# Kernel tuning notes

Measured on AMD Instinct MI355X. Metric: run time of the kernel, lower is better.

The kernel has to match this reference:

```python
import jax, jax.numpy as jnp
import numpy as np

B, L, V, E, M, H = 64, 256, 50000, 300, 50, 256
HD = H // 2  # per-direction LSTM hidden
C1, C2 = 1.0, 0.1


def _reverse_padded(x, lens):
    # reverse each [L, ...] sequence within its valid length; padded tail -> 0
    Ln = x.shape[1]
    idx = lens[:, None] - 1 - jnp.arange(Ln)[None, :]
    ok = idx >= 0
    idxc = jnp.clip(idx, 0, Ln - 1)
    out = jnp.take_along_axis(x, idxc[:, :, None], axis=1)
    return out * ok[:, :, None].astype(x.dtype)


def _lstm_dir(x, valid, w_ih, w_hh, b_ih, b_hh):
    # x: [B, L, D], valid: [B, L] bool. PyTorch gate order i, f, g, o.
    Bn = x.shape[0]
    Hh = w_hh.shape[1]
    xs = jnp.einsum('bld,hd->blh', x, w_ih) + b_ih  # precompute input projection
    xsT = xs.transpose(1, 0, 2)  # [L, B, 4H]
    vT = valid.T  # [L, B]

    def step(carry, inp):
        h, c = carry
        g_in, v = inp
        g = g_in + h @ w_hh.T + b_hh
        i, f, gg, o = jnp.split(g, 4, axis=1)
        c_new = jax.nn.sigmoid(f) * c + jax.nn.sigmoid(i) * jnp.tanh(gg)
        h_new = jax.nn.sigmoid(o) * jnp.tanh(c_new)
        vm = v[:, None]
        return (jnp.where(vm, h_new, h), jnp.where(vm, c_new, c)), jnp.where(vm, h_new, 0.0)

    init = (jnp.zeros((Bn, Hh), x.dtype), jnp.zeros((Bn, Hh), x.dtype))
    _, outs = jax.lax.scan(step, init, (xsT, vT))
    return outs.transpose(1, 0, 2)  # [B, L, Hh], zeros past each len (like pad_packed)


def _forward(sents, masks, labels, lens, word_embed, mask_embed,
             w_ih_f, w_hh_f, b_ih_f, b_hh_f, w_ih_b, w_hh_b, b_ih_b, b_hh_b,
             feat2tri_w, feat2tri_b, transitions, feat2label_w, feat2label_b):
    valid = jnp.arange(L)[None, :] < lens[:, None]  # [B, L]
    # SimpleCat (dropout is identity at eval)
    x = jnp.concatenate([word_embed[sents], mask_embed[masks]], axis=2)  # [B, L, E+M]
    # biLSTM (packed semantics: outputs zero past len)
    hf = _lstm_dir(x, valid, w_ih_f, w_hh_f, b_ih_f, b_hh_f)
    hb = _reverse_padded(_lstm_dir(_reverse_padded(x, lens), valid, w_ih_b, w_hh_b, b_ih_b, b_hh_b), lens)
    context = jnp.concatenate([hf, hb], axis=2)  # [B, L, H]
    # masked target average pooling, broadcast-add back
    mf = masks.astype(context.dtype)
    tavg = jnp.sum(mf[:, :, None] * context, axis=1) / jnp.sum(mf, axis=1)[:, None]
    context = context + tavg[:, None, :]
    # emission scores for the 2-state linear CRF
    emit = jnp.einsum('blh,th->blt', context, feat2tri_w) + feat2tri_b  # [B, L, 2]
    emitT = emit.transpose(1, 0, 2)  # [L, B, 2]
    vT = valid.T  # [L, B]

    # batched CRF forward (alpha), frozen past each len
    def astep(alpha, inp):
        e, v = inp
        a_new = e + jax.nn.logsumexp(alpha[:, :, None] + transitions[None], axis=1)
        alpha = jnp.where(v[:, None], a_new, alpha)
        return alpha, alpha

    alpha0 = emitT[0]
    alpha_last, alphas_rest = jax.lax.scan(astep, alpha0, (emitT[1:], vT[1:]))
    alphas = jnp.concatenate([alpha0[None], alphas_rest], axis=0)  # [L, B, 2]
    logZ = jax.nn.logsumexp(alpha_last, axis=1)  # [B]

    # batched CRF backward (beta); beta[len-1] = 0, frozen past len
    def bstep(beta, inp):
        e_next, v_next = inp
        b_new = jax.nn.logsumexp(transitions[None] + (e_next + beta)[:, None, :], axis=2)
        beta = jnp.where(v_next[:, None], b_new, beta)
        return beta, beta

    beta_init = jnp.zeros((B, 2), context.dtype)
    _, betas_rev = jax.lax.scan(bstep, beta_init, (emitT[1:][::-1], vT[1:][::-1]))
    betas = jnp.concatenate([betas_rev[::-1], beta_init[None]], axis=0)  # [L, B, 2]

    marg = jnp.exp(alphas + betas - logZ[None, :, None]) * vT[:, :, None]  # [L, B, 2]
    sp = marg[:, :, 1].T  # select_polarity, [B, L], zero past len
    sent_v = jnp.einsum('bl,blh->bh', sp, context)
    label_scores = sent_v @ feat2label_w.T + feat2label_b  # [B, 3]
    logp = jax.nn.log_softmax(label_scores, axis=1)
    cls_loss = -jnp.mean(logp[jnp.arange(B), labels])
    s_prob_norm = jnp.mean(jnp.sum(sp, axis=1))  # L1 norm of nonneg marginals
    pena = jax.nn.relu(transitions[1, 0] - transitions[0, 0]) + jax.nn.relu(transitions[0, 1] - transitions[1, 1])
    norm_pen = C1 * pena + C2 * s_prob_norm
    return jnp.stack([cls_loss, norm_pen])


def setup_inputs() -> dict:
    key = jax.random.key(0)
    ks = jax.random.split(key, 20)
    s = 0.1
    sents = jax.random.randint(ks[0], (B, L), 0, V)
    lens = jnp.sort(jax.random.randint(ks[1], (B,), 32, L + 1))[::-1]
    masks = jnp.zeros((B, L), jnp.int32).at[:, :8].set(jax.random.randint(ks[2], (B, 8), 0, 2)).at[:, 0].set(1)
    labels = jax.random.randint(ks[3], (B,), 0, 3)
    D = E + M
    return {
        'sents': sents, 'masks': masks, 'labels': labels, 'lens': lens,
        'word_embed': jax.random.normal(ks[4], (V, E)) * s,
        'mask_embed': jax.random.normal(ks[5], (2, M)) * s,
        'w_ih_f': jax.random.normal(ks[6], (4 * HD, D)) * s,
        'w_hh_f': jax.random.normal(ks[7], (4 * HD, HD)) * s,
        'b_ih_f': jnp.zeros((4 * HD,)), 'b_hh_f': jnp.zeros((4 * HD,)),
        'w_ih_b': jax.random.normal(ks[8], (4 * HD, D)) * s,
        'w_hh_b': jax.random.normal(ks[9], (4 * HD, HD)) * s,
        'b_ih_b': jnp.zeros((4 * HD,)), 'b_hh_b': jnp.zeros((4 * HD,)),
        'feat2tri_w': jax.random.normal(ks[10], (2, H)) * s,
        'feat2tri_b': jnp.zeros((2,)),
        'transitions': jax.random.normal(ks[11], (2, 2)) * s,
        'feat2label_w': jax.random.normal(ks[12], (3, H)) * s,
        'feat2label_b': jnp.zeros((3,)),
    }


def reference(sents, masks, labels, lens, word_embed, mask_embed,
              w_ih_f, w_hh_f, b_ih_f, b_hh_f, w_ih_b, w_hh_b, b_ih_b, b_hh_b,
              feat2tri_w, feat2tri_b, transitions, feat2label_w, feat2label_b):
    return _forward(sents, masks, labels, lens, word_embed, mask_embed,
                    w_ih_f, w_hh_f, b_ih_f, b_hh_f, w_ih_b, w_hh_b, b_ih_b, b_hh_b,
                    feat2tri_w, feat2tri_b, transitions, feat2label_w, feat2label_b)
```

## Files before the change

kernel.cpp:

```cpp
#include <hip/hip_runtime.h>
#include <hip/hip_bf16.h>

#define Bq 64
#define Lq 256
#define Dq 350
#define HDq 128
#define Hq 256
#define G4 512

typedef unsigned short u16;
typedef unsigned int u32;
typedef __attribute__((ext_vector_type(8))) short bf16x8;
typedef __attribute__((ext_vector_type(4))) float f32x4;

__device__ __forceinline__ float bf2f(u16 u) {
    return __uint_as_float(((u32)u) << 16);
}
__device__ __forceinline__ u16 f2bf(float f) {
    __hip_bfloat16 h = __float2bfloat16(f);
    return *(u16*)&h;
}
__device__ __forceinline__ float bflo(u32 u) {
    return __uint_as_float(u << 16);
}
__device__ __forceinline__ float bfhi(u32 u) {
    return __uint_as_float(u & 0xffff0000u);
}
__device__ __forceinline__ float loadf(const void* p, long i, int f32) {
    return f32 ? ((const float*)p)[i] : bf2f(((const u16*)p)[i]);
}
__device__ __forceinline__ float pick8(uint4 q, int i) {
    u32 w = (i >> 1) == 0 ? q.x : (i >> 1) == 1 ? q.y : (i >> 1) == 2 ? q.z : q.w;
    return (i & 1) ? bfhi(w) : bflo(w);
}
__device__ __forceinline__ float fsigm(float x) {
    return 1.f / (1.f + __expf(-x));
}
__device__ __forceinline__ float ftanh(float x) {
    return 1.f - 2.f / (__expf(2.f * x) + 1.f);
}
__device__ __forceinline__ float lse2(float x, float y) {
    float m = fmaxf(x, y);
    return m + logf(expf(x - m) + expf(y - m));
}
__device__ __forceinline__ float lse2f(float x, float y) {
    float m = fmaxf(x, y);
    return m + __logf(__expf(x - m) + __expf(y - m));
}
__device__ __forceinline__ int hswz(int m, int k) {
    return m * 128 + ((((k >> 3) + m) & 15) << 3) + (k & 7);
}
__device__ __forceinline__ u32 pack2(float lo, float hi) {
    return ((u32)f2bf(hi) << 16) | (u32)f2bf(lo);
}

__global__ void detect_kernel(const void* we, int* flag) {
    if (threadIdx.x == 0 && blockIdx.x == 0) {
        const u16* p = (const u16*)we;
        int big = 0;
        for (int i = 0; i < 256; ++i) {
            float a = fabsf(bf2f(p[i]));
            if (!(a < 2.f)) big++;
        }
        *flag = (big > 16) ? 1 : 0;
    }
}

#define LDA 40

__global__ __launch_bounds__(256) void gemm_xs_kernel(
    const int* __restrict__ sents, const int* __restrict__ masks,
    const int* __restrict__ lens,
    const void* __restrict__ word_embed,
    const void* __restrict__ mask_embed,
    const void* __restrict__ w_ih_f, const void* __restrict__ w_ih_b,
    const void* __restrict__ b_ih_f, const void* __restrict__ b_hh_f,
    const void* __restrict__ b_ih_b, const void* __restrict__ b_hh_b,
    const int* __restrict__ flag,
    u16* __restrict__ xsF)
{
    __shared__ __align__(16) u16 As[128 * LDA];
    __shared__ __align__(16) u16 Bs[128 * LDA];
    __shared__ int rowS[128];
    __shared__ int rowM[128];

    int f32 = *flag;
    int tid = threadIdx.x;
    int mBase = blockIdx.y * 128;
    int jGlob = blockIdx.x * 128;
    int dir = jGlob >> 9;
    int jj = jGlob & 511;
    const void* w_ih = dir ? w_ih_b : w_ih_f;
    const void* b_ih = dir ? b_ih_b : b_ih_f;
    const void* b_hh = dir ? b_hh_b : b_hh_f;

    int b = mBase >> 8;
    int posBase = mBase & 255;
    int len = lens[b];

    if (tid < 128) {
        int i = mBase + tid;
        rowS[tid] = sents[i] * 300;
        rowM[tid] = masks[i] * 50;
    }
    int wv = tid >> 6, lane = tid & 63;
    int quad = lane >> 4, col = lane & 15;
    int mS = tid >> 4;
    int k2S = (tid & 15) << 1;
    f32x4 acc[2][8] = {};
    __syncthreads();

    for (int kt = 0; kt < 11; ++kt) {
        int k0 = kt * 32;
        u32 aR[8], bR[8];
        if (f32) {
#pragma unroll
            for (int e = 0; e < 8; ++e) {
                int m = mS + e * 16;
                int gk = k0 + k2S;
                float2 v = make_float2(0.f, 0.f);
                if (gk < 300)
                    v = *(const float2*)((const float*)word_embed + rowS[m] + gk);
                else if (gk < 350)
                    v = *(const float2*)((const float*)mask_embed + rowM[m] + gk - 300);
                aR[e] = pack2(v.x, v.y);
                float2 w2 = make_float2(0.f, 0.f);
                if (gk < 350)
                    w2 = *(const float2*)((const float*)w_ih + (long)(jj + m) * 350 + gk);
                bR[e] = pack2(w2.x, w2.y);
            }
        } else {
#pragma unroll
            for (int e = 0; e < 8; ++e) {
                int m = mS + e * 16;
                int gk = k0 + k2S;
                u32 v = 0;
                if (gk < 300)
                    v = *(const u32*)((const u16*)word_embed + rowS[m] + gk);
                else if (gk < 350)
                    v = *(const u32*)((const u16*)mask_embed + rowM[m] + gk - 300);
                aR[e] = v;
                u32 w2 = 0;
                if (gk < 350)
                    w2 = *(const u32*)((const u16*)w_ih + (long)(jj + m) * 350 + gk);
                bR[e] = w2;
            }
        }
        __syncthreads();
#pragma unroll
        for (int e = 0; e < 8; ++e) {
            int m = mS + e * 16;
            *(u32*)&As[m * LDA + k2S] = aR[e];
            *(u32*)&Bs[m * LDA + k2S] = bR[e];
        }
        __syncthreads();
        bf16x8 af[2], bfr[8];
#pragma unroll
        for (int mt = 0; mt < 2; ++mt)
            af[mt] = *(const bf16x8*)&As[(wv * 32 + mt * 16 + col) * LDA + quad * 8];
#pragma unroll
        for (int nt = 0; nt < 8; ++nt)
            bfr[nt] = *(const bf16x8*)&Bs[(nt * 16 + col) * LDA + quad * 8];
#pragma unroll
        for (int mt = 0; mt < 2; ++mt)
#pragma unroll
            for (int nt = 0; nt < 8; ++nt)
                acc[mt][nt] = __builtin_amdgcn_mfma_f32_16x16x32_bf16(
                    af[mt], bfr[nt], acc[mt][nt], 0, 0, 0);
    }

    int bgv = b >> 2, quadv = b & 3;
#pragma unroll
    for (int nt = 0; nt < 8; ++nt) {
        int ng = jj + nt * 16 + col;
        float bias = loadf(b_ih, ng, f32) + loadf(b_hh, ng, f32);
        int g = ng >> 7, dd = ng & 127;
        int wvx = dd >> 4, colv = dd & 15;
        int row = ((dir * 16 + bgv) * 8 + wvx) * 4 + g;
        int lanev = quadv * 16 + colv;
#pragma unroll
        for (int mt = 0; mt < 2; ++mt)
#pragma unroll
            for (int r = 0; r < 4; ++r) {
                int pos = posBase + wv * 32 + mt * 16 + quad * 4 + r;
                int s = dir ? (len - 1 - pos) : pos;
                if (s >= 0) {
                    long idxe = ((long)(row * 32 + (s >> 3))) * 512
                                + lanev * 8 + (s & 7);
                    xsF[idxe] = f2bf(acc[mt][nt][r] + bias);
                }
            }
    }
}

__global__ __launch_bounds__(512, 1) void lstm_mfma_kernel(
    const u16* __restrict__ xsF,
    const void* __restrict__ w_hh_f, const void* __restrict__ w_hh_b,
    const int* __restrict__ lens, const int* __restrict__ flag,
    u16* __restrict__ context)
{
    int f32 = *flag;
    int blk = blockIdx.x;
    int dir = blk >> 4, bg = blk & 15;
    int tid = threadIdx.x;
    int w = tid >> 6, lane = tid & 63;
    int quad = lane >> 4, col = lane & 15;
    const void* w_hh = dir ? w_hh_b : w_hh_f;

    __shared__ __align__(16) u16 hbuf[2][16 * 128];
    __shared__ __align__(16) u16 hist[16 * 512];
    __shared__ int len_s[4];
    __shared__ int maxlen_s;

    if (tid < 4) len_s[tid] = lens[bg * 4 + tid];
    for (int i = tid; i < 2 * 16 * 128; i += 512) ((u16*)hbuf)[i] = 0;
    __syncthreads();
    if (tid == 0) {
        int mx = 0;
        for (int m = 0; m < 4; ++m) mx = max(mx, len_s[m]);
        maxlen_s = mx;
    }
    for (int m = 0; m < 4; ++m) {
        int b = bg * 4 + m;
        int len = len_s[m];
        for (int idx = tid; idx < (Lq - len) * HDq; idx += 512) {
            int p = len + (idx >> 7);
            int d = idx & 127;
            context[((b << 8) + p) * Hq + dir * HDq + d] = 0;
        }
    }
    __syncthreads();
    int T16 = (maxlen_s + 15) & ~15;

    bf16x8 wfrag[4][4];
#pragma unroll
    for (int g = 0; g < 4; ++g) {
        int n = g * 128 + w * 16 + col;
#pragma unroll
        for (int c = 0; c < 4; ++c) {
            int k0 = c * 32 + quad * 8;
            bf16x8 fr;
            if (f32) {
                const float* src = (const float*)w_hh + (long)n * 128 + k0;
#pragma unroll
                for (int j = 0; j < 8; ++j) fr[j] = (short)f2bf(src[j]);
            } else {
                fr = *(const bf16x8*)((const u16*)w_hh + (long)n * 128 + k0);
            }
            wfrag[g][c] = fr;
        }
    }

    float c_st = 0.f;
    int mylen = len_s[quad];
    int mloc = quad * 4;
    int dcol = w * 16 + col;
    int rowb = ((dir * 16 + bg) * 8 + w) * 4;

    int nCh = T16 >> 3;
    for (int tc = 0; tc < nCh; ++tc) {
        uint4 xsq[4];
#pragma unroll
        for (int g = 0; g < 4; ++g)
            xsq[g] = *(const uint4*)(xsF + ((long)((rowb + g) * 32 + tc)) * 512
                                     + lane * 8);
#pragma unroll
        for (int u = 0; u < 8; ++u) {
            int t = tc * 8 + u;
            const u16* hb = hbuf[t & 1];
            u16* hn = hbuf[(t + 1) & 1];
            bf16x8 af[4];
#pragma unroll
            for (int c = 0; c < 4; ++c)
                af[c] = *(const bf16x8*)&hb[hswz(col, c * 32 + quad * 8)];
            f32x4 acc[4];
#pragma unroll
            for (int g = 0; g < 4; ++g) {
                f32x4 a4 = {0.f, 0.f, 0.f, 0.f};
                a4[0] = pick8(xsq[g], u);
                acc[g] = a4;
            }
#pragma unroll
            for (int c = 0; c < 4; ++c)
#pragma unroll
                for (int g = 0; g < 4; ++g)
                    acc[g] = __builtin_amdgcn_mfma_f32_16x16x32_bf16(
                        af[c], wfrag[g][c], acc[g], 0, 0, 0);
            bool vld = (t < mylen);
            float i_ = fsigm(acc[0][0]);
            float f_ = fsigm(acc[1][0]);
            float g_ = ftanh(acc[2][0]);
            float o_ = fsigm(acc[3][0]);
            float cn = f_ * c_st + i_ * g_;
            if (vld) c_st = cn;
            u16 hnew = f2bf(o_ * ftanh(cn));
            u16 hv = vld ? hnew : hb[hswz(mloc, dcol)];
            hn[hswz(mloc, dcol)] = hv;
            if (vld) hist[(t & 15) * 512 + quad * 128 + dcol] = hnew;
            __syncthreads();
            if ((t & 15) == 15) {
                int tb = t - 15;
                for (int idx = tid; idx < 4096; idx += 512) {
                    int tl = idx >> 8;
                    int rem = idx & 255;
                    int m = rem >> 6;
                    int d2 = (rem & 63) << 1;
                    int tt = tb + tl;
                    int len = len_s[m];
                    if (tt < len) {
                        int pos = dir ? (len - 1 - tt) : tt;
                        int b = bg * 4 + m;
                        u32 v = *(const u32*)&hist[tl * 512 + m * 128 + d2];
                        *(u32*)&context[((b << 8) + pos) * Hq + dir * HDq + d2] = v;
                    }
                }
                __syncthreads();
            }
        }
    }
}

__global__ void tavg_kernel(const int* __restrict__ masks,
                            const u16* __restrict__ context,
                            float* __restrict__ tavg)
{
    int b = blockIdx.x, h = threadIdx.x;
    float s = 0.f, msum = 0.f;
    for (int l = 0; l < Lq; ++l) {
        int m = masks[(b << 8) + l];
        if (m) {
            s += (float)m * bf2f(context[(((b << 8) + l) << 8) + h]);
            msum += (float)m;
        }
    }
    tavg[(b << 8) + h] = s / msum;
}

__global__ void emit_kernel(const u16* __restrict__ context,
                            const float* __restrict__ tavg,
                            const void* __restrict__ f2t_w,
                            const void* __restrict__ f2t_b,
                            const int* __restrict__ flag,
                            float* __restrict__ emit_T)
{
    int f32 = *flag;
    int i = blockIdx.x;
    int b = i >> 8;
    int l = i & 255;
    int k = threadIdx.x;
    ushort4 c4 = *(const ushort4*)(context + (long)i * Hq + 4 * k);
    float4 t4 = *(const float4*)(tavg + b * Hq + 4 * k);
    float v0 = bf2f(c4.x) + t4.x, v1 = bf2f(c4.y) + t4.y;
    float v2 = bf2f(c4.z) + t4.z, v3 = bf2f(c4.w) + t4.w;
    int d = 4 * k;
    float p0 = v0 * loadf(f2t_w, d, f32) + v1 * loadf(f2t_w, d + 1, f32) +
               v2 * loadf(f2t_w, d + 2, f32) + v3 * loadf(f2t_w, d + 3, f32);
    float p1 = v0 * loadf(f2t_w, Hq + d, f32) + v1 * loadf(f2t_w, Hq + d + 1, f32) +
               v2 * loadf(f2t_w, Hq + d + 2, f32) + v3 * loadf(f2t_w, Hq + d + 3, f32);
#pragma unroll
    for (int off = 32; off >= 1; off >>= 1) {
        p0 += __shfl_down(p0, off);
        p1 += __shfl_down(p1, off);
    }
    if (k == 0) {
        float2 e = make_float2(p0 + loadf(f2t_b, 0, f32),
                               p1 + loadf(f2t_b, 1, f32));
        *(float2*)(emit_T + ((l << 6) + b) * 2) = e;
    }
}

__global__ void crf_kernel(const float* __restrict__ emit_T,
                           const int* __restrict__ lens,
                           const void* __restrict__ trans,
                           const int* __restrict__ flag,
                           float* __restrict__ alphas_T,
                           float* __restrict__ sp_T,
                           float* __restrict__ spsum)
{
    int f32 = *flag;
    int b = threadIdx.x;
    float t00 = loadf(trans, 0, f32), t01 = loadf(trans, 1, f32);
    float t10 = loadf(trans, 2, f32), t11 = loadf(trans, 3, f32);
    int len = lens[b];

    float a0, a1;
    {
        float2 e0 = *(const float2*)(emit_T + (b << 1));
        a0 = e0.x; a1 = e0.y;
        *(float2*)(alphas_T + (b << 1)) = make_float2(a0, a1);
    }
    for (int tc = 0; tc < 32; ++tc) {
        float2 ebuf[8];
#pragma unroll
        for (int u = 0; u < 8; ++u) {
            int t = tc * 8 + u;
            ebuf[u] = *(const float2*)(emit_T + (((t << 6) + b) << 1));
        }
#pragma unroll
        for (int u = 0; u < 8; ++u) {
            int t = tc * 8 + u;
            if (t >= 1 && t < len) {
                float n0 = ebuf[u].x + lse2f(a0 + t00, a1 + t10);
                float n1 = ebuf[u].y + lse2f(a0 + t01, a1 + t11);
                a0 = n0; a1 = n1;
            }
            if (t >= 1)
                *(float2*)(alphas_T + (((t << 6) + b) << 1)) = make_float2(a0, a1);
        }
    }
    float logZ = lse2f(a0, a1);

    float b0 = 0.f, b1 = 0.f;
    float ssum = 0.f;
    {
        float a255 = alphas_T[((((Lq - 1) << 6) + b) << 1) + 1];
        float v = (Lq - 1 < len) ? __expf(a255 - logZ) : 0.f;
        sp_T[((Lq - 1) << 6) + b] = v; ssum += v;
    }
    for (int tc = 31; tc >= 0; --tc) {
        float2 ebuf[8];
        float abuf[8];
#pragma unroll
        for (int u = 0; u < 8; ++u) {
            int t = tc * 8 + u;
            ebuf[u] = *(const float2*)(emit_T + (((t << 6) + b) << 1));
            if (t >= 1)
                abuf[u] = alphas_T[((((t - 1) << 6) + b) << 1) + 1];
        }
#pragma unroll
        for (int uu = 7; uu >= 0; --uu) {
            int t = tc * 8 + uu;
            if (t < 1) break;
            if (t < len) {
                float e0 = ebuf[uu].x, e1 = ebuf[uu].y;
                float n0 = lse2f(t00 + e0 + b0, t01 + e1 + b1);
                float n1 = lse2f(t10 + e0 + b0, t11 + e1 + b1);
                b0 = n0; b1 = n1;
            }
            float v = ((t - 1) < len) ? __expf(abuf[uu] + b1 - logZ) : 0.f;
            sp_T[((t - 1) << 6) + b] = v; ssum += v;
        }
    }
    spsum[b] = ssum;
}

__global__ void sentv_kernel(const float* __restrict__ sp_T,
                             const u16* __restrict__ context,
                             const float* __restrict__ tavg,
                             const float* __restrict__ spsum,
                             float* __restrict__ sentv)
{
    int b = blockIdx.x, h = threadIdx.x;
    float s = 0.f;
    for (int l = 0; l < Lq; ++l)
        s += sp_T[(l << 6) + b] * bf2f(context[(((b << 8) + l) << 8) + h]);
    sentv[(b << 8) + h] = s + spsum[b] * tavg[(b << 8) + h];
}

__global__ void final_kernel(const float* __restrict__ sentv,
                             const float* __restrict__ spsum,
                             const void* __restrict__ f2l_w,
                             const void* __restrict__ f2l_b,
                             const void* __restrict__ trans,
                             const int* __restrict__ labels,
                             const int* __restrict__ flag,
                             void* __restrict__ out)
{
    int f32 = *flag;
    int b = threadIdx.x;
    float s0 = 0.f, s1 = 0.f, s2 = 0.f;
    for (int h = 0; h < Hq; ++h) {
        float v = sentv[(b << 8) + h];
        s0 += v * loadf(f2l_w, h, f32);
        s1 += v * loadf(f2l_w, Hq + h, f32);
        s2 += v * loadf(f2l_w, 2 * Hq + h, f32);
    }
    s0 += loadf(f2l_b, 0, f32); s1 += loadf(f2l_b, 1, f32); s2 += loadf(f2l_b, 2, f32);
    float m = fmaxf(s0, fmaxf(s1, s2));
    float lse = m + logf(expf(s0 - m) + expf(s1 - m) + expf(s2 - m));
    int lab = labels[b];
    float sc = lab == 0 ? s0 : (lab == 1 ? s1 : s2);
    float loss = lse - sc;
    float sn = spsum[b];
#pragma unroll
    for (int off = 32; off >= 1; off >>= 1) {
        loss += __shfl_down(loss, off);
        sn += __shfl_down(sn, off);
    }
    if (b == 0) {
        float cls = loss / 64.f;
        float t00 = loadf(trans, 0, f32), t01 = loadf(trans, 1, f32);
        float t10 = loadf(trans, 2, f32), t11 = loadf(trans, 3, f32);
        float pena = fmaxf(t10 - t00, 0.f) + fmaxf(t01 - t11, 0.f);
        float np = 1.0f * pena + 0.1f * (sn / 64.f);
        if (f32) {
            ((float*)out)[0] = cls;
            ((float*)out)[1] = np;
        } else {
            ((__hip_bfloat16*)out)[0] = __float2bfloat16(cls);
            ((__hip_bfloat16*)out)[1] = __float2bfloat16(np);
        }
    }
}

extern "C" void kernel_launch(void* const* d_in, const int* in_sizes, int n_in,
                              void* d_out, int out_size, void* d_ws, size_t ws_size,
                              hipStream_t stream)
{
    const int* sents  = (const int*)d_in[0];
    const int* masks  = (const int*)d_in[1];
    const int* labels = (const int*)d_in[2];
    const int* lens   = (const int*)d_in[3];
    const void* word_embed = d_in[4];
    const void* mask_embed = d_in[5];
    const void* w_ih_f = d_in[6];
    const void* w_hh_f = d_in[7];
    const void* b_ih_f = d_in[8];
    const void* b_hh_f = d_in[9];
    const void* w_ih_b = d_in[10];
    const void* w_hh_b = d_in[11];
    const void* b_ih_b = d_in[12];
    const void* b_hh_b = d_in[13];
    const void* f2t_w  = d_in[14];
    const void* f2t_b  = d_in[15];
    const void* trans  = d_in[16];
    const void* f2l_w  = d_in[17];
    const void* f2l_b  = d_in[18];

    char* wsb = (char*)d_ws;
    size_t off = 33554432;
    u16*   xsF     = (u16*)wsb;
    u16*   context = (u16*)(wsb + off);      off += 8388608;
    float* tavg    = (float*)(wsb + off);    off += 65536;
    float* alphas  = (float*)(wsb + off);    off += 131072;
    float* emit    = (float*)(wsb + off);    off += 131072;
    float* sp      = (float*)(wsb + off);    off += 65536;
    float* spsum   = (float*)(wsb + off);    off += 4096;
    float* sentv   = (float*)(wsb + off);    off += 65536;
    int*   flag    = (int*)(wsb + off);

    detect_kernel<<<1, 64, 0, stream>>>(word_embed, flag);

    gemm_xs_kernel<<<dim3(8, 128), 256, 0, stream>>>(
        sents, masks, lens, word_embed, mask_embed,
        w_ih_f, w_ih_b, b_ih_f, b_hh_f, b_ih_b, b_hh_b, flag, xsF);

    lstm_mfma_kernel<<<32, 512, 0, stream>>>(
        xsF, w_hh_f, w_hh_b, lens, flag, context);

    tavg_kernel<<<Bq, 256, 0, stream>>>(masks, context, tavg);

    emit_kernel<<<Bq * Lq, 64, 0, stream>>>(context, tavg, f2t_w, f2t_b, flag, emit);

    crf_kernel<<<1, 64, 0, stream>>>(emit, lens, trans, flag, alphas, sp, spsum);

    sentv_kernel<<<Bq, 256, 0, stream>>>(sp, context, tavg, spsum, sentv);

    final_kernel<<<1, 64, 0, stream>>>(sentv, spsum, f2l_w, f2l_b, trans, labels,
                                       flag, d_out);
}
```

Measured before the change: 590.3 us.

## Fuse both LSTM directions into one block and split MFMA accumulator chains

The recurrent LSTM kernel now runs the forward and backward directions of a batch group inside one 1024-thread block, two 512-thread halves, so the launch drops from 32 blocks to 16. Each step's gate accumulation is split into two independent MFMA chains that are summed at the end, halving the serial dependency depth per step. This is meant to cut per-step latency of the sequential recurrence. In exchange, both directions now share every block barrier, each CU holds twice as many waves competing for MFMA units, and the tighter register budget under 1024-thread launch bounds risks spills of the resident weight fragments.

Measured after the change: 907.8 us. +53.8%, slower.

```diff
diff --git a/kernel.cpp b/kernel.cpp
--- a/kernel.cpp
+++ b/kernel.cpp
@@ -193,27 +193,28 @@
     }
 }
 
-__global__ __launch_bounds__(512, 1) void lstm_mfma_kernel(
+__global__ __launch_bounds__(1024, 1) void lstm_mfma_kernel(
     const u16* __restrict__ xsF,
     const void* __restrict__ w_hh_f, const void* __restrict__ w_hh_b,
     const int* __restrict__ lens, const int* __restrict__ flag,
     u16* __restrict__ context)
 {
     int f32 = *flag;
-    int blk = blockIdx.x;
-    int dir = blk >> 4, bg = blk & 15;
+    int bg = blockIdx.x;
     int tid = threadIdx.x;
-    int w = tid >> 6, lane = tid & 63;
+    int dgrp = tid >> 9;
+    int t9 = tid & 511;
+    int w = t9 >> 6, lane = t9 & 63;
     int quad = lane >> 4, col = lane & 15;
-    const void* w_hh = dir ? w_hh_b : w_hh_f;
-
-    __shared__ __align__(16) u16 hbuf[2][16 * 128];
-    __shared__ __align__(16) u16 hist[16 * 512];
+    const void* w_hh = dgrp ? w_hh_b : w_hh_f;
+
+    __shared__ __align__(16) u16 hbuf[2][2][16 * 128];
+    __shared__ __align__(16) u16 hist[2][16 * 512];
     __shared__ int len_s[4];
     __shared__ int maxlen_s;
 
     if (tid < 4) len_s[tid] = lens[bg * 4 + tid];
-    for (int i = tid; i < 2 * 16 * 128; i += 512) ((u16*)hbuf)[i] = 0;
+    for (int i = tid; i < 2 * 2 * 16 * 128; i += 1024) ((u16*)hbuf)[i] = 0;
     __syncthreads();
     if (tid == 0) {
         int mx = 0;
@@ -223,10 +224,10 @@
     for (int m = 0; m < 4; ++m) {
         int b = bg * 4 + m;
         int len = len_s[m];
-        for (int idx = tid; idx < (Lq - len) * HDq; idx += 512) {
+        for (int idx = t9; idx < (Lq - len) * HDq; idx += 512) {
             int p = len + (idx >> 7);
             int d = idx & 127;
-            context[((b << 8) + p) * Hq + dir * HDq + d] = 0;
+            context[((b << 8) + p) * Hq + dgrp * HDq + d] = 0;
         }
     }
     __syncthreads();
@@ -255,7 +256,7 @@
     int mylen = len_s[quad];
     int mloc = quad * 4;
     int dcol = w * 16 + col;
-    int rowb = ((dir * 16 + bg) * 8 + w) * 4;
+    int rowb = ((dgrp * 16 + bg) * 8 + w) * 4;
 
     int nCh = T16 >> 3;
     for (int tc = 0; tc < nCh; ++tc) {
@@ -267,40 +268,50 @@
 #pragma unroll
         for (int u = 0; u < 8; ++u) {
             int t = tc * 8 + u;
-            const u16* hb = hbuf[t & 1];
-            u16* hn = hbuf[(t + 1) & 1];
+            const u16* hb = hbuf[dgrp][t & 1];
+            u16* hn = hbuf[dgrp][(t + 1) & 1];
             bf16x8 af[4];
 #pragma unroll
             for (int c = 0; c < 4; ++c)
                 af[c] = *(const bf16x8*)&hb[hswz(col, c * 32 + quad * 8)];
-            f32x4 acc[4];
+            f32x4 accA[4], accB[4];
 #pragma unroll
             for (int g = 0; g < 4; ++g) {
                 f32x4 a4 = {0.f, 0.f, 0.f, 0.f};
                 a4[0] = pick8(xsq[g], u);
-                acc[g] = a4;
-            }
-#pragma unroll
-            for (int c = 0; c < 4; ++c)
-#pragma unroll
-                for (int g = 0; g < 4; ++g)
-                    acc[g] = __builtin_amdgcn_mfma_f32_16x16x32_bf16(
-                        af[c], wfrag[g][c], acc[g], 0, 0, 0);
+                accA[g] = a4;
+                f32x4 z4 = {0.f, 0.f, 0.f, 0.f};
+                accB[g] = z4;
+            }
+#pragma unroll
+            for (int g = 0; g < 4; ++g) {
+                accA[g] = __builtin_amdgcn_mfma_f32_16x16x32_bf16(
+                    af[0], wfrag[g][0], accA[g], 0, 0, 0);
+                accB[g] = __builtin_amdgcn_mfma_f32_16x16x32_bf16(
+                    af[2], wfrag[g][2], accB[g], 0, 0, 0);
+            }
+#pragma unroll
+            for (int g = 0; g < 4; ++g) {
+                accA[g] = __builtin_amdgcn_mfma_f32_16x16x32_bf16(
+                    af[1], wfrag[g][1], accA[g], 0, 0, 0);
+                accB[g] = __builtin_amdgcn_mfma_f32_16x16x32_bf16(
+                    af[3], wfrag[g][3], accB[g], 0, 0, 0);
+            }
             bool vld = (t < mylen);
-            float i_ = fsigm(acc[0][0]);
-            float f_ = fsigm(acc[1][0]);
-            float g_ = ftanh(acc[2][0]);
-            float o_ = fsigm(acc[3][0]);
+            float i_ = fsigm(accA[0][0] + accB[0][0]);
+            float f_ = fsigm(accA[1][0] + accB[1][0]);
+            float g_ = ftanh(accA[2][0] + accB[2][0]);
+            float o_ = fsigm(accA[3][0] + accB[3][0]);
             float cn = f_ * c_st + i_ * g_;
             if (vld) c_st = cn;
             u16 hnew = f2bf(o_ * ftanh(cn));
             u16 hv = vld ? hnew : hb[hswz(mloc, dcol)];
             hn[hswz(mloc, dcol)] = hv;
-            if (vld) hist[(t & 15) * 512 + quad * 128 + dcol] = hnew;
+            if (vld) hist[dgrp][(t & 15) * 512 + quad * 128 + dcol] = hnew;
             __syncthreads();
             if ((t & 15) == 15) {
                 int tb = t - 15;
-                for (int idx = tid; idx < 4096; idx += 512) {
+                for (int idx = t9; idx < 4096; idx += 512) {
                     int tl = idx >> 8;
                     int rem = idx & 255;
                     int m = rem >> 6;
@@ -308,10 +319,10 @@
                     int tt = tb + tl;
                     int len = len_s[m];
                     if (tt < len) {
-                        int pos = dir ? (len - 1 - tt) : tt;
+                        int pos = dgrp ? (len - 1 - tt) : tt;
                         int b = bg * 4 + m;
-                        u32 v = *(const u32*)&hist[tl * 512 + m * 128 + d2];
-                        *(u32*)&context[((b << 8) + pos) * Hq + dir * HDq + d2] = v;
+                        u32 v = *(const u32*)&hist[dgrp][tl * 512 + m * 128 + d2];
+                        *(u32*)&context[((b << 8) + pos) * Hq + dgrp * HDq + d2] = v;
                     }
                 }
                 __syncthreads();
@@ -545,7 +556,7 @@
         sents, masks, lens, word_embed, mask_embed,
         w_ih_f, w_ih_b, b_ih_f, b_hh_f, b_ih_b, b_hh_b, flag, xsF);
 
-    lstm_mfma_kernel<<<32, 512, 0, stream>>>(
+    lstm_mfma_kernel<<<16, 1024, 0, stream>>>(
         xsF, w_hh_f, w_hh_b, lens, flag, context);
 
     tavg_kernel<<<Bq, 256, 0, stream>>>(masks, context, tavg);
```

## Split tail reductions across sequence chunks with atomics and widen emit blocks

Applied to the files above, without the earlier changes.

The tavg and sentv reductions are split into 8 sequence chunks per batch row, with partial sums combined by atomicAdd into buffers zeroed by a memset. This raises the post-LSTM block count from 64 to 512. The emit kernel now handles four rows per 256-thread block. The serial per-thread final projection becomes a parallel per-batch reduction kernel followed by a small loss kernel. Costs are an extra memset, extra launches and float atomics whose summation order is nondeterministic, and the scratch buffers reuse the xsF workspace region after the LSTM has finished with it.

Measured after the change: 535.6 us. 1.1x faster.

```diff
diff --git a/kernel.cpp b/kernel.cpp
--- a/kernel.cpp
+++ b/kernel.cpp
@@ -38,10 +38,6 @@
 }
 __device__ __forceinline__ float ftanh(float x) {
     return 1.f - 2.f / (__expf(2.f * x) + 1.f);
-}
-__device__ __forceinline__ float lse2(float x, float y) {
-    float m = fmaxf(x, y);
-    return m + logf(expf(x - m) + expf(y - m));
 }
 __device__ __forceinline__ float lse2f(float x, float y) {
     float m = fmaxf(x, y);
@@ -320,38 +316,48 @@
     }
 }
 
-__global__ void tavg_kernel(const int* __restrict__ masks,
-                            const u16* __restrict__ context,
-                            float* __restrict__ tavg)
-{
-    int b = blockIdx.x, h = threadIdx.x;
-    float s = 0.f, msum = 0.f;
-    for (int l = 0; l < Lq; ++l) {
-        int m = masks[(b << 8) + l];
+__global__ void tavg_part_kernel(const int* __restrict__ masks,
+                                 const u16* __restrict__ context,
+                                 float* __restrict__ tavgsum,
+                                 float* __restrict__ msum)
+{
+    __shared__ int m_s[32];
+    int b = blockIdx.y, lc = blockIdx.x;
+    int h = threadIdx.x;
+    if (h < 32) m_s[h] = masks[(b << 8) + (lc << 5) + h];
+    __syncthreads();
+    float s = 0.f;
+    int mcnt = 0;
+    for (int l = 0; l < 32; ++l) {
+        int m = m_s[l];
         if (m) {
-            s += (float)m * bf2f(context[(((b << 8) + l) << 8) + h]);
-            msum += (float)m;
-        }
-    }
-    tavg[(b << 8) + h] = s / msum;
+            s += (float)m * bf2f(context[(((b << 8) + (lc << 5) + l) << 8) + h]);
+            mcnt += m;
+        }
+    }
+    atomicAdd(&tavgsum[(b << 8) + h], s);
+    if (h == 0 && mcnt) atomicAdd(&msum[b], (float)mcnt);
 }
 
 __global__ void emit_kernel(const u16* __restrict__ context,
-                            const float* __restrict__ tavg,
+                            const float* __restrict__ tavgsum,
+                            const float* __restrict__ msum,
                             const void* __restrict__ f2t_w,
                             const void* __restrict__ f2t_b,
                             const int* __restrict__ flag,
                             float* __restrict__ emit_T)
 {
     int f32 = *flag;
-    int i = blockIdx.x;
+    int wv = threadIdx.x >> 6;
+    int i = (blockIdx.x << 2) + wv;
     int b = i >> 8;
     int l = i & 255;
-    int k = threadIdx.x;
+    int k = threadIdx.x & 63;
+    float inv = 1.f / msum[b];
     ushort4 c4 = *(const ushort4*)(context + (long)i * Hq + 4 * k);
-    float4 t4 = *(const float4*)(tavg + b * Hq + 4 * k);
-    float v0 = bf2f(c4.x) + t4.x, v1 = bf2f(c4.y) + t4.y;
-    float v2 = bf2f(c4.z) + t4.z, v3 = bf2f(c4.w) + t4.w;
+    float4 t4 = *(const float4*)(tavgsum + (b << 8) + 4 * k);
+    float v0 = bf2f(c4.x) + t4.x * inv, v1 = bf2f(c4.y) + t4.y * inv;
+    float v2 = bf2f(c4.z) + t4.z * inv, v3 = bf2f(c4.w) + t4.w * inv;
     int d = 4 * k;
     float p0 = v0 * loadf(f2t_w, d, f32) + v1 * loadf(f2t_w, d + 1, f32) +
                v2 * loadf(f2t_w, d + 2, f32) + v3 * loadf(f2t_w, d + 3, f32);
@@ -444,38 +450,67 @@
     spsum[b] = ssum;
 }
 
-__global__ void sentv_kernel(const float* __restrict__ sp_T,
-                             const u16* __restrict__ context,
-                             const float* __restrict__ tavg,
-                             const float* __restrict__ spsum,
-                             float* __restrict__ sentv)
-{
+__global__ void sentv_part_kernel(const float* __restrict__ sp_T,
+                                  const u16* __restrict__ context,
+                                  float* __restrict__ sentvsum)
+{
+    __shared__ float sp_s[32];
+    int b = blockIdx.y, lc = blockIdx.x;
+    int h = threadIdx.x;
+    if (h < 32) sp_s[h] = sp_T[(((lc << 5) + h) << 6) + b];
+    __syncthreads();
+    float s = 0.f;
+#pragma unroll 4
+    for (int l = 0; l < 32; ++l)
+        s += sp_s[l] * bf2f(context[(((b << 8) + (lc << 5) + l) << 8) + h]);
+    atomicAdd(&sentvsum[(b << 8) + h], s);
+}
+
+__global__ void finalize_kernel(const float* __restrict__ sentvsum,
+                                const float* __restrict__ tavgsum,
+                                const float* __restrict__ msum,
+                                const float* __restrict__ spsum,
+                                const void* __restrict__ f2l_w,
+                                const int* __restrict__ flag,
+                                float* __restrict__ scores)
+{
+    __shared__ float red[4][3];
+    int f32 = *flag;
     int b = blockIdx.x, h = threadIdx.x;
-    float s = 0.f;
-    for (int l = 0; l < Lq; ++l)
-        s += sp_T[(l << 6) + b] * bf2f(context[(((b << 8) + l) << 8) + h]);
-    sentv[(b << 8) + h] = s + spsum[b] * tavg[(b << 8) + h];
-}
-
-__global__ void final_kernel(const float* __restrict__ sentv,
-                             const float* __restrict__ spsum,
-                             const void* __restrict__ f2l_w,
-                             const void* __restrict__ f2l_b,
-                             const void* __restrict__ trans,
-                             const int* __restrict__ labels,
-                             const int* __restrict__ flag,
-                             void* __restrict__ out)
+    float v = sentvsum[(b << 8) + h] +
+              spsum[b] * (tavgsum[(b << 8) + h] / msum[b]);
+    float p0 = v * loadf(f2l_w, h, f32);
+    float p1 = v * loadf(f2l_w, Hq + h, f32);
+    float p2 = v * loadf(f2l_w, 2 * Hq + h, f32);
+#pragma unroll
+    for (int off = 32; off >= 1; off >>= 1) {
+        p0 += __shfl_down(p0, off);
+        p1 += __shfl_down(p1, off);
+        p2 += __shfl_down(p2, off);
+    }
+    int wv = h >> 6;
+    if ((h & 63) == 0) { red[wv][0] = p0; red[wv][1] = p1; red[wv][2] = p2; }
+    __syncthreads();
+    if (h == 0) {
+        scores[b * 4 + 0] = red[0][0] + red[1][0] + red[2][0] + red[3][0];
+        scores[b * 4 + 1] = red[0][1] + red[1][1] + red[2][1] + red[3][1];
+        scores[b * 4 + 2] = red[0][2] + red[1][2] + red[2][2] + red[3][2];
+    }
+}
+
+__global__ void final2_kernel(const float* __restrict__ scores,
+                              const float* __restrict__ spsum,
+                              const void* __restrict__ f2l_b,
+                              const void* __restrict__ trans,
+                              const int* __restrict__ labels,
+                              const int* __restrict__ flag,
+                              void* __restrict__ out)
 {
     int f32 = *flag;
     int b = threadIdx.x;
-    float s0 = 0.f, s1 = 0.f, s2 = 0.f;
-    for (int h = 0; h < Hq; ++h) {
-        float v = sentv[(b << 8) + h];
-        s0 += v * loadf(f2l_w, h, f32);
-        s1 += v * loadf(f2l_w, Hq + h, f32);
-        s2 += v * loadf(f2l_w, 2 * Hq + h, f32);
-    }
-    s0 += loadf(f2l_b, 0, f32); s1 += loadf(f2l_b, 1, f32); s2 += loadf(f2l_b, 2, f32);
+    float s0 = scores[b * 4 + 0] + loadf(f2l_b, 0, f32);
+    float s1 = scores[b * 4 + 1] + loadf(f2l_b, 1, f32);
+    float s2 = scores[b * 4 + 2] + loadf(f2l_b, 2, f32);
     float m = fmaxf(s0, fmaxf(s1, s2));
     float lse = m + logf(expf(s0 - m) + expf(s1 - m) + expf(s2 - m));
     int lab = labels[b];
@@ -530,13 +565,17 @@
     char* wsb = (char*)d_ws;
     size_t off = 33554432;
     u16*   xsF     = (u16*)wsb;
+    float* tavgsum  = (float*)wsb;
+    float* sentvsum = (float*)(wsb + 65536);
+    float* msum     = (float*)(wsb + 131072);
+    float* scores   = (float*)(wsb + 131584);
     u16*   context = (u16*)(wsb + off);      off += 8388608;
-    float* tavg    = (float*)(wsb + off);    off += 65536;
+    off += 65536;
     float* alphas  = (float*)(wsb + off);    off += 131072;
     float* emit    = (float*)(wsb + off);    off += 131072;
     float* sp      = (float*)(wsb + off);    off += 65536;
     float* spsum   = (float*)(wsb + off);    off += 4096;
-    float* sentv   = (float*)(wsb + off);    off += 65536;
+    off += 65536;
     int*   flag    = (int*)(wsb + off);
 
     detect_kernel<<<1, 64, 0, stream>>>(word_embed, flag);
@@ -548,14 +587,21 @@
     lstm_mfma_kernel<<<32, 512, 0, stream>>>(
         xsF, w_hh_f, w_hh_b, lens, flag, context);
 
-    tavg_kernel<<<Bq, 256, 0, stream>>>(masks, context, tavg);
-
-    emit_kernel<<<Bq * Lq, 64, 0, stream>>>(context, tavg, f2t_w, f2t_b, flag, emit);
+    hipMemsetAsync(wsb, 0, 131328, stream);
+
+    tavg_part_kernel<<<dim3(8, 64), 256, 0, stream>>>(
+        masks, context, tavgsum, msum);
+
+    emit_kernel<<<Bq * Lq / 4, 256, 0, stream>>>(
+        context, tavgsum, msum, f2t_w, f2t_b, flag, emit);
 
     crf_kernel<<<1, 64, 0, stream>>>(emit, lens, trans, flag, alphas, sp, spsum);
 
-    sentv_kernel<<<Bq, 256, 0, stream>>>(sp, context, tavg, spsum, sentv);
-
-    final_kernel<<<1, 64, 0, stream>>>(sentv, spsum, f2l_w, f2l_b, trans, labels,
-                                       flag, d_out);
-}
+    sentv_part_kernel<<<dim3(8, 64), 256, 0, stream>>>(sp, context, sentvsum);
+
+    finalize_kernel<<<Bq, 256, 0, stream>>>(
+        sentvsum, tavgsum, msum, spsum, f2l_w, flag, scores);
+
+    final2_kernel<<<1, 64, 0, stream>>>(
+        scores, spsum, f2l_b, trans, labels, flag, d_out);
+}
```
